# Kernel tuning notes

Measured on AMD Instinct MI355X. Metric: run time of the kernel, lower is better.

Reference implementation:

```python
import jax, jax.numpy as jnp
import numpy as np
from jax import lax

HEADS = 4
DIM = 64
GATE_HID = 16


def setup_inputs() -> dict:
    key = jax.random.key(0)
    ks = jax.random.split(key, 12)
    b, c, h, w = 2, DIM, 48, 48
    s = 0.05
    x = jax.random.normal(ks[0], (b, c, h, w), jnp.float32)
    Wqkv = jax.random.normal(ks[1], (3 * c, c), jnp.float32) * s
    bqkv = jax.random.normal(ks[2], (3 * c,), jnp.float32) * s
    Wpos = jax.random.normal(ks[3], (3 * c, 1, 3, 3), jnp.float32) * s
    bpos = jax.random.normal(ks[4], (3 * c,), jnp.float32) * s
    Wg1 = jax.random.normal(ks[5], (GATE_HID, 1), jnp.float32) * 0.5
    bg1 = jax.random.normal(ks[6], (GATE_HID,), jnp.float32) * 0.1
    Wg2 = jax.random.normal(ks[7], (1, GATE_HID), jnp.float32) * 0.5
    bg2 = jax.random.normal(ks[8], (1,), jnp.float32) * 0.1
    Wproj = jax.random.normal(ks[9], (c, c), jnp.float32) * s
    bproj = jax.random.normal(ks[10], (c,), jnp.float32) * s
    return {"x": x, "Wqkv": Wqkv, "bqkv": bqkv, "Wpos": Wpos, "bpos": bpos,
            "Wg1": Wg1, "bg1": bg1, "Wg2": Wg2, "bg2": bg2,
            "Wproj": Wproj, "bproj": bproj}


def _forward(x, Wqkv, bqkv, Wpos, bpos, Wg1, bg1, Wg2, bg2, Wproj, bproj):
    b, c, h, w = x.shape
    n = h * w
    heads = HEADS
    hd = c // heads
    scale = hd ** -0.5
    # qkv 1x1 conv then 3x3 depthwise positional conv
    qkv = jnp.einsum('bchw,oc->bohw', x, Wqkv) + bqkv[None, :, None, None]
    qkv = lax.conv_general_dilated(
        qkv, Wpos, window_strides=(1, 1), padding='SAME',
        feature_group_count=3 * c,
        dimension_numbers=('NCHW', 'OIHW', 'NCHW')) + bpos[None, :, None, None]
    q, k, v = jnp.split(qkv, 3, axis=1)

    def to_heads(t):
        # [b,c,h,w] -> [b,heads,n,hd]
        return t.reshape(b, c, n).transpose(0, 2, 1).reshape(b, n, heads, hd).transpose(0, 2, 1, 3)

    q, k, v = to_heads(q), to_heads(k), to_heads(v)
    attn = jnp.einsum('bhid,bhjd->bhij', q, k) * scale  # [b,heads,n,n]
    prob = jax.nn.softmax(attn, axis=-1)
    entropy = -(prob * jnp.log(jnp.clip(prob, 1e-12))).sum(-1).mean(-1)  # [b,heads]
    # entropy gate: sigmoid(fc2(relu(fc1(e)))) * 0.9 + 0.1
    hgate = jax.nn.relu(entropy[..., None] @ Wg1.T + bg1)  # [b,heads,16]
    ratio = jax.nn.sigmoid(hgate @ Wg2.T + bg2)[..., 0] * 0.9 + 0.1  # [b,heads]
    # dynamic per-(batch,head) top-k along rows via rank threshold
    keep = jnp.clip(jnp.ceil(ratio * n).astype(jnp.int32), 1, n)  # [b,heads]
    sorted_desc = -jnp.sort(-attn, axis=-1)  # [b,heads,n,n]
    idx = jnp.broadcast_to((keep - 1)[:, :, None, None], (b, heads, n, 1))
    thresh = jnp.take_along_axis(sorted_desc, idx, axis=-1)  # [b,heads,n,1]
    sparse = jnp.where(attn >= thresh, attn, -jnp.inf)
    p = jax.nn.softmax(sparse, axis=-1)
    out = jnp.einsum('bhij,bhjd->bhid', p, v)  # [b,heads,n,hd]
    out = out.transpose(0, 2, 1, 3).reshape(b, n, c)
    out = out @ Wproj.T + bproj
    return out.transpose(0, 2, 1).reshape(b, c, h, w)


def reference(x, Wqkv, bqkv, Wpos, bpos, Wg1, bg1, Wg2, bg2, Wproj, bproj):
    return _forward(x, Wqkv, bqkv, Wpos, bpos, Wg1, bg1, Wg2, bg2, Wproj, bproj)
```

## Files before the change

kernel.cpp:

```cpp
#include <hip/hip_runtime.h>
#include <hip/hip_fp16.h>


typedef _Float16 half8_t __attribute__((ext_vector_type(8)));
typedef float floatx4 __attribute__((ext_vector_type(4)));

union HU { unsigned short s; _Float16 h; };
__device__ __forceinline__ _Float16 ubits_h(unsigned short u) {
  HU c; c.s = u; return c.h;
}
__device__ __forceinline__ _Float16 key_h(unsigned k) {
  unsigned short u = (k & 0x8000u) ? (unsigned short)(k & 0x7FFFu)
                                   : (unsigned short)((~k) & 0xFFFFu);
  return ubits_h(u);
}

__global__ __launch_bounds__(256) void k_qkv(const float* __restrict__ x,
                                             const float* __restrict__ W,
                                             const float* __restrict__ bias,
                                             float* __restrict__ out,
                                             float* __restrict__ ent) {
  if (blockIdx.x == 0 && threadIdx.x < 8) ent[threadIdx.x] = 0.f;
  int blk = blockIdx.x;
  int chunk = blk % 9;
  int og = (blk / 9) % 48;
  int b = blk / (9 * 48);
  int o0 = og * 4;
  int pos = chunk * 256 + threadIdx.x;
  const float* xb = x + b * 64 * 2304 + pos;
  const float* w0 = W + (o0 + 0) * 64;
  const float* w1 = W + (o0 + 1) * 64;
  const float* w2 = W + (o0 + 2) * 64;
  const float* w3 = W + (o0 + 3) * 64;
  float a0 = bias[o0 + 0], a1 = bias[o0 + 1];
  float a2 = bias[o0 + 2], a3 = bias[o0 + 3];
#pragma unroll
  for (int c = 0; c < 64; c++) {
    float xv = xb[c * 2304];
    a0 = fmaf(w0[c], xv, a0);
    a1 = fmaf(w1[c], xv, a1);
    a2 = fmaf(w2[c], xv, a2);
    a3 = fmaf(w3[c], xv, a3);
  }
  out[(b * 192 + o0 + 0) * 2304 + pos] = a0;
  out[(b * 192 + o0 + 1) * 2304 + pos] = a1;
  out[(b * 192 + o0 + 2) * 2304 + pos] = a2;
  out[(b * 192 + o0 + 3) * 2304 + pos] = a3;
}

__global__ __launch_bounds__(256) void k_dw(const float* __restrict__ qkv,
                                            const float* __restrict__ Wpos,
                                            const float* __restrict__ bpos,
                                            _Float16* __restrict__ q2,
                                            _Float16* __restrict__ k2,
                                            _Float16* __restrict__ vt) {
  __shared__ float smem[8][384];
  int blk = blockIdx.x;
  int chunk = blk % 9;
  int half = (blk / 9) % 2;
  int sel = (blk / 18) % 3;
  int head = (blk / 54) % 4;
  int b = blk / 216;
  int chbase = sel * 64 + head * 16 + half * 8;
  int bh = b * 4 + head;
  int tid = threadIdx.x;
  int p0 = chunk * 256;
  int baserow = p0 / 48;
  int rA = min(max(baserow - 1, 0), 40);

  const float* src = qkv + (size_t)(b * 192 + chbase) * 2304;
#pragma unroll
  for (int l = 0; l < 12; l++) {
    int idx = tid + l * 256;
    int ch = idx / 384;
    int off = idx - ch * 384;
    int rr = off / 48;
    int cc = off - rr * 48;
    smem[ch][off] = src[(size_t)ch * 2304 + (rA + rr) * 48 + cc];
  }
  __syncthreads();

  int pos = p0 + tid;
  int yy = pos / 48, xx = pos - yy * 48;
  int ry = yy - rA;
  float accv[8];
#pragma unroll
  for (int d = 0; d < 8; d++) {
    const float* w = Wpos + (chbase + d) * 9;
    float a = bpos[chbase + d];
#pragma unroll
    for (int dy = -1; dy <= 1; dy++) {
      int y2 = yy + dy;
      if ((unsigned)y2 < 48u) {
#pragma unroll
        for (int dx = -1; dx <= 1; dx++) {
          int x2 = xx + dx;
          if ((unsigned)x2 < 48u)
            a = fmaf(w[(dy + 1) * 3 + (dx + 1)], smem[d][(ry + dy) * 48 + x2],
                     a);
        }
      }
    }
    accv[d] = a;
  }

  if (sel == 2) {
#pragma unroll
    for (int d = 0; d < 8; d++)
      vt[((size_t)bh * 16 + half * 8 + d) * 2304 + pos] = (_Float16)accv[d];
  } else {
    _Float16 h1[8], h2[8];
#pragma unroll
    for (int d = 0; d < 8; d++) {
      float a = (sel == 0) ? accv[d] * 0.25f : accv[d];
      h1[d] = (_Float16)a;
      h2[d] = (_Float16)(a - (float)h1[d]);
    }
    _Float16* dst = ((sel == 0) ? q2 : k2) + ((size_t)bh * 2304 + pos) * 32;
    *(uint4*)(dst + half * 8) = *(uint4*)&h1[0];
    *(uint4*)(dst + 16 + half * 8) = *(uint4*)&h2[0];
  }
}

template <bool STORE>
__global__ __launch_bounds__(256) void k_ent_t(const _Float16* __restrict__ q2,
                                               const _Float16* __restrict__ k2,
                                               float* __restrict__ ent,
                                               _Float16* __restrict__ lgH) {
  __shared__ __align__(16) _Float16 tBuf[4][16][72];
  __shared__ float sWv[4][16], uWv[4][16];

  int blk = blockIdx.x;
  int rowtile = blk % 144;
  int bh = blk / 144;
  int row0 = rowtile * 16;
  int tid = threadIdx.x, lane = tid & 63, wave = tid >> 6;
  int m16 = lane & 15, quad = lane >> 4;

  const half8_t* q2v =
      (const half8_t*)(q2 + ((size_t)bh * 2304 + row0 + m16) * 32);
  half8_t A1 = q2v[quad];
  half8_t zh = {};
  half8_t A2 = (lane < 32) ? A1 : zh;
  const half8_t* kbase = (const half8_t*)(k2 + (size_t)bh * 2304 * 32);

  float s[4] = {0.f, 0.f, 0.f, 0.f}, u[4] = {0.f, 0.f, 0.f, 0.f};
  for (int g = 0; g < 9; g++) {
#pragma unroll
    for (int tt = 0; tt < 4; tt++) {
      int t = g * 4 + tt;
      int col = wave * 576 + t * 16 + m16;
      const half8_t* kk = kbase + (size_t)col * 4;
      half8_t b1 = kk[quad & 1];
      half8_t b2 = kk[2 + (quad & 1)];
      floatx4 acc = {};
      acc = __builtin_amdgcn_mfma_f32_16x16x32_f16(A2, b2, acc, 0, 0, 0);
      acc = __builtin_amdgcn_mfma_f32_16x16x32_f16(A1, b1, acc, 0, 0, 0);
#pragma unroll
      for (int i = 0; i < 4; i++) {
        if (STORE) tBuf[wave][quad * 4 + i][tt * 16 + m16] = (_Float16)acc[i];
        float e = __expf(acc[i]);
        s[i] += e;
        u[i] = fmaf(acc[i], e, u[i]);
      }
    }
    if (STORE) {
      __syncthreads();
      int rb = lane >> 3, seg = lane & 7;
#pragma unroll
      for (int it = 0; it < 2; it++) {
        int rr = it * 8 + rb;
        uint4 vv = *(const uint4*)&tBuf[wave][rr][seg * 8];
        *(uint4*)(lgH + ((size_t)bh * 2304 + row0 + rr) * 2304 + wave * 576 +
                  g * 64 + seg * 8) = vv;
      }
      __syncthreads();
    }
  }
#pragma unroll
  for (int off = 1; off < 16; off <<= 1) {
#pragma unroll
    for (int i = 0; i < 4; i++) {
      s[i] += __shfl_xor(s[i], off);
      u[i] += __shfl_xor(u[i], off);
    }
  }
  if (m16 == 0) {
#pragma unroll
    for (int i = 0; i < 4; i++) {
      sWv[wave][quad * 4 + i] = s[i];
      uWv[wave][quad * 4 + i] = u[i];
    }
  }
  __syncthreads();
  if (tid < 16) {
    float S = sWv[0][tid] + sWv[1][tid] + sWv[2][tid] + sWv[3][tid];
    float U = uWv[0][tid] + uWv[1][tid] + uWv[2][tid] + uWv[3][tid];
    float er = __logf(S) - U / S;
    er += __shfl_xor(er, 1);
    er += __shfl_xor(er, 2);
    er += __shfl_xor(er, 4);
    er += __shfl_xor(er, 8);
    if (tid == 0) atomicAdd(&ent[bh], er);
  }
}

__global__ __launch_bounds__(512, 6) void k_attn_f(
    const _Float16* __restrict__ q2, const _Float16* __restrict__ k2,
    const _Float16* __restrict__ vt, const float* __restrict__ ent,
    const float* __restrict__ Wg1, const float* __restrict__ bg1,
    const float* __restrict__ Wg2, const float* __restrict__ bg2,
    float* __restrict__ oh) {
  __shared__ __align__(16) _Float16 lg[8 * 2320];
  __shared__ float sS[8];
  __shared__ __align__(16) float redSh[8][64];

  int blk = blockIdx.x;
  int bh = blk & 7;
  int tile = blk >> 3;
  int row0 = tile * 8;
  int tid = threadIdx.x, lane = tid & 63, wave = tid >> 6;
  int m16 = lane & 15, quad = lane >> 4;

  float eAvg = ent[bh] * (1.f / 2304.f);
  float gacc = bg2[0];
#pragma unroll
  for (int i = 0; i < 16; i++) {
    float h = fmaxf(fmaf(eAvg, Wg1[i], bg1[i]), 0.f);
    gacc = fmaf(h, Wg2[i], gacc);
  }
  float ratio = 0.9f / (1.f + __expf(-gacc)) + 0.1f;
  int kp = (int)ceilf(ratio * 2304.f);
  unsigned keep = (unsigned)min(max(kp, 1), 2304);

  {
    const half8_t* q2v =
        (const half8_t*)(q2 + ((size_t)bh * 2304 + row0 + (m16 & 7)) * 32);
    half8_t A1 = q2v[quad];
    half8_t zh = {};
    half8_t A2 = (lane < 32) ? A1 : zh;
    const half8_t* kbase = (const half8_t*)(k2 + (size_t)bh * 2304 * 32);
#pragma unroll 2
    for (int t = 0; t < 18; t++) {
      int col = wave * 288 + t * 16 + m16;
      const half8_t* kk = kbase + (size_t)col * 4;
      half8_t b1 = kk[quad & 1];
      half8_t b2 = kk[2 + (quad & 1)];
      floatx4 acc = {};
      acc = __builtin_amdgcn_mfma_f32_16x16x32_f16(A2, b2, acc, 0, 0, 0);
      acc = __builtin_amdgcn_mfma_f32_16x16x32_f16(A1, b1, acc, 0, 0, 0);
      if (quad < 2) {
#pragma unroll
        for (int i = 0; i < 4; i++)
          lg[(quad * 4 + i) * 2320 + col] = (_Float16)acc[i];
      }
    }
  }
  __syncthreads();

  {
    char* rb = (char*)lg + wave * 4640;
    const uint4* s4 = (const uint4*)rb;
    uint4 q0 = s4[lane];
    uint4 q1 = s4[lane + 64];
    uint4 q2r = s4[lane + 128];
    uint4 q3 = s4[lane + 192];
    uint2 q4 = *(const uint2*)(rb + 4096 + lane * 8);
    unsigned wb[18] = {q0.x, q0.y, q0.z, q0.w, q1.x, q1.y, q1.z, q1.w,
                       q2r.x, q2r.y, q2r.z, q2r.w, q3.x, q3.y, q3.z, q3.w,
                       q4.x, q4.y};
    unsigned ku[36];
#pragma unroll
    for (int i = 0; i < 18; i++) {
      unsigned kbi =
          wb[i] ^ (((wb[i] >> 15) & 0x00010001u) * 0x7FFFu + 0x80008000u);
      ku[2 * i + 0] = kbi & 0xFFFFu;
      ku[2 * i + 1] = kbi >> 16;
    }

    unsigned T = 0u;
    for (int bit = 15; bit >= 0; --bit) {
      unsigned cand = T | (1u << bit);
      unsigned cnt = 0u;
#pragma unroll
      for (int i = 0; i < 36; i++)
        cnt += (unsigned)__popcll(__ballot(ku[i] >= cand));
      if (cnt >= keep) {
        T = cand;
        if (cnt == keep) break;
      }
    }
    _Float16 th_h = key_h(T);

    float sp = 0.f;
    uint4* prow4 = (uint4*)rb;
#pragma unroll
    for (int g = 0; g < 4; g++) {
      uint4 o;
      unsigned ow[4];
#pragma unroll
      for (int wj = 0; wj < 4; wj++) {
        unsigned w = wb[g * 4 + wj];
        _Float16 hlo = ubits_h((unsigned short)(w & 0xFFFFu));
        _Float16 hhi = ubits_h((unsigned short)(w >> 16));
        float plo = (hlo >= th_h) ? __expf((float)hlo) : 0.f;
        float phi = (hhi >= th_h) ? __expf((float)hhi) : 0.f;
        __half2 hp = __floats2half2_rn(plo, phi);
        ow[wj] = *(unsigned*)&hp;
        if (wj == 0) sp += ((plo + phi));
      }
      o.x = ow[0]; o.y = ow[1]; o.z = ow[2]; o.w = ow[3];
      prow4[lane + g * 64] = o;
      {
        _Float16 h2a = ubits_h((unsigned short)(wb[g * 4 + 1] & 0xFFFFu));
        _Float16 h2b = ubits_h((unsigned short)(wb[g * 4 + 1] >> 16));
        _Float16 h3a = ubits_h((unsigned short)(wb[g * 4 + 2] & 0xFFFFu));
        _Float16 h3b = ubits_h((unsigned short)(wb[g * 4 + 2] >> 16));
        _Float16 h4a = ubits_h((unsigned short)(wb[g * 4 + 3] & 0xFFFFu));
        _Float16 h4b = ubits_h((unsigned short)(wb[g * 4 + 3] >> 16));
        float p2 = (h2a >= th_h) ? __expf((float)h2a) : 0.f;
        float p3 = (h2b >= th_h) ? __expf((float)h2b) : 0.f;
        float p4 = (h3a >= th_h) ? __expf((float)h3a) : 0.f;
        float p5 = (h3b >= th_h) ? __expf((float)h3b) : 0.f;
        float p6 = (h4a >= th_h) ? __expf((float)h4a) : 0.f;
        float p7 = (h4b >= th_h) ? __expf((float)h4b) : 0.f;
        sp += (p2 + p3);
        sp += (p4 + p5) + (p6 + p7);
      }
    }
    {
      _Float16 h0 = ubits_h((unsigned short)(wb[16] & 0xFFFFu));
      _Float16 h1 = ubits_h((unsigned short)(wb[16] >> 16));
      _Float16 h2 = ubits_h((unsigned short)(wb[17] & 0xFFFFu));
      _Float16 h3 = ubits_h((unsigned short)(wb[17] >> 16));
      float p0 = (h0 >= th_h) ? __expf((float)h0) : 0.f;
      float p1 = (h1 >= th_h) ? __expf((float)h1) : 0.f;
      float p2 = (h2 >= th_h) ? __expf((float)h2) : 0.f;
      float p3 = (h3 >= th_h) ? __expf((float)h3) : 0.f;
      sp += (p0 + p1) + (p2 + p3);
      uint2 o;
      __half2 hp0 = __floats2half2_rn(p0, p1); o.x = *(unsigned*)&hp0;
      __half2 hp1 = __floats2half2_rn(p2, p3); o.y = *(unsigned*)&hp1;
      *(uint2*)(rb + 4096 + lane * 8) = o;
    }
#pragma unroll
    for (int off = 1; off < 64; off <<= 1) sp += __shfl_xor(sp, off);
    if (lane == 0) sS[wave] = sp;
  }
  __syncthreads();

  {
    int g = wave >> 2;
    int jq = wave & 3;
    const _Float16* vrow = vt + ((size_t)bh * 16 + m16) * 2304;
    const _Float16* prow = lg + (size_t)(g * 4 + (m16 & 3)) * 2320;
    int jb0 = jq * 576 + quad * 8;
    floatx4 acc = {};
#pragma unroll 6
    for (int t = 0; t < 18; t++) {
      int jb = jb0 + t * 32;
      half8_t a2 = *(const half8_t*)&prow[jb];
      half8_t b2 = *(const half8_t*)&vrow[jb];
      acc = __builtin_amdgcn_mfma_f32_16x16x32_f16(a2, b2, acc, 0, 0, 0);
    }
    if (lane < 16) {
      *(floatx4*)&redSh[wave][m16 * 4] = acc;
    }
  }
  __syncthreads();
  if (tid < 128) {
    int g = tid >> 6, idx = tid & 63;
    int r = idx & 3, d = idx >> 2;
    float s2 = redSh[g * 4 + 0][d * 4 + r] + redSh[g * 4 + 1][d * 4 + r] +
               redSh[g * 4 + 2][d * 4 + r] + redSh[g * 4 + 3][d * 4 + r];
    oh[((size_t)(bh * 2304 + row0 + g * 4 + r)) * 16 + d] =
        s2 / sS[g * 4 + r];
  }
}

__global__ __launch_bounds__(256) void k_proj(const float* __restrict__ oh,
                                              const float* __restrict__ Wp,
                                              const float* __restrict__ bp,
                                              float* __restrict__ out) {
  int blk = blockIdx.x;
  int chunk = blk % 9;
  int cog = (blk / 9) % 16;
  int b = blk / (9 * 16);
  int co0 = cog * 4;
  int pos = chunk * 256 + threadIdx.x;
  float a0 = bp[co0 + 0], a1 = bp[co0 + 1], a2 = bp[co0 + 2], a3 = bp[co0 + 3];
#pragma unroll
  for (int head = 0; head < 4; head++) {
    const float4* op =
        (const float4*)(oh + ((size_t)((b * 4 + head) * 2304 + pos)) * 16);
#pragma unroll
    for (int p = 0; p < 4; p++) {
      float4 o4 = op[p];
#pragma unroll
      for (int i = 0; i < 4; i++) {
        const float* wr = Wp + (co0 + i) * 64 + head * 16 + p * 4;
        float* ai = (i == 0) ? &a0 : ((i == 1) ? &a1 : ((i == 2) ? &a2 : &a3));
        *ai = fmaf(wr[0], o4.x, *ai);
        *ai = fmaf(wr[1], o4.y, *ai);
        *ai = fmaf(wr[2], o4.z, *ai);
        *ai = fmaf(wr[3], o4.w, *ai);
      }
    }
  }
  out[(b * 64 + co0 + 0) * 2304 + pos] = a0;
  out[(b * 64 + co0 + 1) * 2304 + pos] = a1;
  out[(b * 64 + co0 + 2) * 2304 + pos] = a2;
  out[(b * 64 + co0 + 3) * 2304 + pos] = a3;
}

extern "C" void kernel_launch(void* const* d_in, const int* in_sizes, int n_in,
                              void* d_out, int out_size, void* d_ws,
                              size_t ws_size, hipStream_t stream) {
  const float* x    = (const float*)d_in[0];
  const float* Wqkv = (const float*)d_in[1];
  const float* bqkv = (const float*)d_in[2];
  const float* Wpos = (const float*)d_in[3];
  const float* bpos = (const float*)d_in[4];
  const float* Wg1  = (const float*)d_in[5];
  const float* bg1  = (const float*)d_in[6];
  const float* Wg2  = (const float*)d_in[7];
  const float* bg2  = (const float*)d_in[8];
  const float* Wpr  = (const float*)d_in[9];
  const float* bpr  = (const float*)d_in[10];
  float* out = (float*)d_out;

  char* base = (char*)d_ws;
  float* qkv_raw = (float*)base;
  float* oh = qkv_raw + 884736;
  float* ent = oh + 294912;
  _Float16* q2 = (_Float16*)(ent + 8);
  _Float16* k2 = q2 + 589824;
  _Float16* vt = k2 + 589824;

  hipLaunchKernelGGL(k_qkv, dim3(2 * 48 * 9), dim3(256), 0, stream,
                     x, Wqkv, bqkv, qkv_raw, ent);
  hipLaunchKernelGGL(k_dw, dim3(432), dim3(256), 0, stream,
                     qkv_raw, Wpos, bpos, q2, k2, vt);
  hipLaunchKernelGGL((k_ent_t<false>), dim3(8 * 144), dim3(256), 0, stream,
                     q2, k2, ent, (_Float16*)nullptr);
  hipLaunchKernelGGL(k_attn_f, dim3(2304), dim3(512), 0, stream,
                     q2, k2, vt, ent, Wg1, bg1, Wg2, bg2, oh);
  hipLaunchKernelGGL(k_proj, dim3(2 * 16 * 9), dim3(256), 0, stream,
                     oh, Wpr, bpr, out);
}
```

Measured before the change: 228.4 us.

## Process 16 query rows per attention block to fill the MFMA tile

```diff
diff --git a/kernel.cpp b/kernel.cpp
--- a/kernel.cpp
+++ b/kernel.cpp
@@ -4,6 +4,8 @@
 
 typedef _Float16 half8_t __attribute__((ext_vector_type(8)));
 typedef float floatx4 __attribute__((ext_vector_type(4)));
+
+#define LSTR 2328
 
 union HU { unsigned short s; _Float16 h; };
 __device__ __forceinline__ _Float16 ubits_h(unsigned short u) {
@@ -205,20 +207,19 @@
   }
 }
 
-__global__ __launch_bounds__(512, 6) void k_attn_f(
+__global__ __launch_bounds__(512, 4) void k_attn_f(
     const _Float16* __restrict__ q2, const _Float16* __restrict__ k2,
     const _Float16* __restrict__ vt, const float* __restrict__ ent,
     const float* __restrict__ Wg1, const float* __restrict__ bg1,
     const float* __restrict__ Wg2, const float* __restrict__ bg2,
     float* __restrict__ oh) {
-  __shared__ __align__(16) _Float16 lg[8 * 2320];
-  __shared__ float sS[8];
-  __shared__ __align__(16) float redSh[8][64];
+  __shared__ __align__(16) _Float16 lg[16 * LSTR];
+  __shared__ float sS[16];
 
   int blk = blockIdx.x;
   int bh = blk & 7;
   int tile = blk >> 3;
-  int row0 = tile * 8;
+  int row0 = tile * 16;
   int tid = threadIdx.x, lane = tid & 63, wave = tid >> 6;
   int m16 = lane & 15, quad = lane >> 4;
 
@@ -235,7 +236,7 @@
 
   {
     const half8_t* q2v =
-        (const half8_t*)(q2 + ((size_t)bh * 2304 + row0 + (m16 & 7)) * 32);
+        (const half8_t*)(q2 + ((size_t)bh * 2304 + row0 + m16) * 32);
     half8_t A1 = q2v[quad];
     half8_t zh = {};
     half8_t A2 = (lane < 32) ? A1 : zh;
@@ -249,17 +250,17 @@
       floatx4 acc = {};
       acc = __builtin_amdgcn_mfma_f32_16x16x32_f16(A2, b2, acc, 0, 0, 0);
       acc = __builtin_amdgcn_mfma_f32_16x16x32_f16(A1, b1, acc, 0, 0, 0);
-      if (quad < 2) {
-#pragma unroll
-        for (int i = 0; i < 4; i++)
-          lg[(quad * 4 + i) * 2320 + col] = (_Float16)acc[i];
-      }
-    }
-  }
-  __syncthreads();
-
-  {
-    char* rb = (char*)lg + wave * 4640;
+#pragma unroll
+      for (int i = 0; i < 4; i++)
+        lg[(quad * 4 + i) * LSTR + col] = (_Float16)acc[i];
+    }
+  }
+  __syncthreads();
+
+#pragma unroll 1
+  for (int rr = 0; rr < 2; rr++) {
+    int r = wave * 2 + rr;
+    char* rb = (char*)lg + (size_t)r * (LSTR * 2);
     const uint4* s4 = (const uint4*)rb;
     uint4 q0 = s4[lane];
     uint4 q1 = s4[lane + 64];
@@ -345,17 +346,15 @@
     }
 #pragma unroll
     for (int off = 1; off < 64; off <<= 1) sp += __shfl_xor(sp, off);
-    if (lane == 0) sS[wave] = sp;
-  }
-  __syncthreads();
-
-  {
-    int g = wave >> 2;
-    int jq = wave & 3;
+    if (lane == 0) sS[r] = sp;
+  }
+  __syncthreads();
+
+  floatx4 acc = {};
+  if (wave < 4) {
     const _Float16* vrow = vt + ((size_t)bh * 16 + m16) * 2304;
-    const _Float16* prow = lg + (size_t)(g * 4 + (m16 & 3)) * 2320;
-    int jb0 = jq * 576 + quad * 8;
-    floatx4 acc = {};
+    const _Float16* prow = lg + (size_t)m16 * LSTR;
+    int jb0 = wave * 576 + quad * 8;
 #pragma unroll 6
     for (int t = 0; t < 18; t++) {
       int jb = jb0 + t * 32;
@@ -363,18 +362,21 @@
       half8_t b2 = *(const half8_t*)&vrow[jb];
       acc = __builtin_amdgcn_mfma_f32_16x16x32_f16(a2, b2, acc, 0, 0, 0);
     }
-    if (lane < 16) {
-      *(floatx4*)&redSh[wave][m16 * 4] = acc;
-    }
-  }
-  __syncthreads();
-  if (tid < 128) {
-    int g = tid >> 6, idx = tid & 63;
-    int r = idx & 3, d = idx >> 2;
-    float s2 = redSh[g * 4 + 0][d * 4 + r] + redSh[g * 4 + 1][d * 4 + r] +
-               redSh[g * 4 + 2][d * 4 + r] + redSh[g * 4 + 3][d * 4 + r];
-    oh[((size_t)(bh * 2304 + row0 + g * 4 + r)) * 16 + d] =
-        s2 / sS[g * 4 + r];
+  }
+  __syncthreads();
+  float* red = (float*)lg;
+  if (wave < 4) {
+#pragma unroll
+    for (int i = 0; i < 4; i++)
+      red[wave * 256 + (quad * 4 + i) * 16 + m16] = acc[i];
+  }
+  __syncthreads();
+  if (tid < 256) {
+    int r = tid >> 4;
+    float s2 = red[0 * 256 + tid] + red[1 * 256 + tid] +
+               red[2 * 256 + tid] + red[3 * 256 + tid];
+    int d = tid & 15;
+    oh[((size_t)(bh * 2304 + row0 + r)) * 16 + d] = s2 / sS[r];
   }
 }
 
@@ -443,7 +445,7 @@
                      qkv_raw, Wpos, bpos, q2, k2, vt);
   hipLaunchKernelGGL((k_ent_t<false>), dim3(8 * 144), dim3(256), 0, stream,
                      q2, k2, ent, (_Float16*)nullptr);
-  hipLaunchKernelGGL(k_attn_f, dim3(2304), dim3(512), 0, stream,
+  hipLaunchKernelGGL(k_attn_f, dim3(1152), dim3(512), 0, stream,
                      q2, k2, vt, ent, Wg1, bg1, Wg2, bg2, oh);
   hipLaunchKernelGGL(k_proj, dim3(2 * 16 * 9), dim3(256), 0, stream,
                      oh, Wpr, bpr, out);
```

Measured after the change: 208.5 us. 8.7% less time.
